# Kernel optimization log

Measured on AMD Instinct MI355X. Metric: run time of the kernel, lower is better.

## Reference

```python
import jax, jax.numpy as jnp
import numpy as np

N_NODES = 100000
NEG_SLOPE = 0.2


def gat_conv(x, W, att_src, att_dst, bias, src, dst, heads, out_ch):
    # x: [N, F_in]; W: [F_in, heads*out_ch]; att_*: [heads, out_ch]; bias: [heads*out_ch]
    N = x.shape[0]
    h = (x @ W).reshape(N, heads, out_ch)                 # [N, H, C]
    a_src = jnp.sum(h * att_src[None], axis=-1)           # [N, H]
    a_dst = jnp.sum(h * att_dst[None], axis=-1)           # [N, H]
    # per-edge unnormalized attention logits (PyG GATConv)
    alpha = jax.nn.leaky_relu(a_src[src] + a_dst[dst], NEG_SLOPE)   # [E, H]
    # scatter-softmax over edges grouped by destination node
    m = jax.ops.segment_max(alpha, dst, num_segments=N)   # [N, H]
    m = jnp.where(jnp.isfinite(m), m, 0.0)
    e = jnp.exp(alpha - m[dst])                           # [E, H]
    s = jax.ops.segment_sum(e, dst, num_segments=N)       # [N, H]
    alpha = e / (s[dst] + 1e-16)
    # weighted scatter-add aggregation of neighbor features
    out = jax.ops.segment_sum(alpha[:, :, None] * h[src], dst, num_segments=N)  # [N, H, C]
    return out.reshape(N, heads * out_ch) + bias


def setup_inputs() -> dict:
    key = jax.random.key(0)
    ks = jax.random.split(key, 10)
    F_in = 128
    x = jax.random.normal(ks[0], (N_NODES, F_in), dtype=jnp.float32)
    edge_index = jax.random.randint(ks[1], (2, 3200000), 0, N_NODES, dtype=jnp.int64)
    g = 0.1
    return {
        "x": x,
        "edge_index": edge_index,
        "W1": jax.random.normal(ks[2], (F_in, 32), jnp.float32) * g,
        "att_src1": jax.random.normal(ks[3], (2, 16), jnp.float32) * g,
        "att_dst1": jax.random.normal(ks[4], (2, 16), jnp.float32) * g,
        "b1": jnp.zeros((32,), jnp.float32),
        "W2": jax.random.normal(ks[5], (32, 2), jnp.float32) * g,
        "att_src2": jax.random.normal(ks[6], (1, 2), jnp.float32) * g,
        "att_dst2": jax.random.normal(ks[7], (1, 2), jnp.float32) * g,
        "b2": jnp.zeros((2,), jnp.float32),
    }


def reference(x, edge_index, W1, att_src1, att_dst1, b1, W2, att_src2, att_dst2, b2):
    N = x.shape[0]
    # add self-loops (PyG GATConv default add_self_loops=True)
    loops = jnp.arange(N, dtype=edge_index.dtype)
    src = jnp.concatenate([edge_index[0], loops])
    dst = jnp.concatenate([edge_index[1], loops])
    h = gat_conv(x, W1, att_src1, att_dst1, b1, src, dst, heads=2, out_ch=16)
    h = jax.nn.elu(h)
    h = gat_conv(h, W2, att_src2, att_dst2, b2, src, dst, heads=1, out_ch=2)
    return jax.nn.log_softmax(h, axis=1)
```

## Files before the change

### kernel.cpp

```cpp
#include <hip/hip_runtime.h>
#include <hip/hip_bf16.h>
#include <hip/hip_fp16.h>

#define LEAK   0.2f
#define NPB    200
#define CAP    8192
#define CAPSH  13
#define SBITS  17
#define SMASK  0x1FFFF
#define CHUNKB 8192

__device__ __forceinline__ unsigned pkh(float a, float b) {
    __half2 h = __floats2half2_rn(a, b);
    return *(unsigned*)&h;
}
__device__ __forceinline__ float2 uph(unsigned u) {
    __half2 h = *(__half2*)&u;
    return __half22float2(h);
}

__global__ __launch_bounds__(512) void kbin(const int* __restrict__ ei, int E, int K,
                                            int* __restrict__ cursor,
                                            int* __restrict__ binned) {
    __shared__ int hist[512], gb[512], lbase[512], lcur[512];
    __shared__ unsigned short rbk[CHUNKB];
    __shared__ int sv[CHUNKB];
    __shared__ int swt[8];
    __shared__ int probe;
    int t = threadIdx.x;
    hist[t] = 0;
    if (t == 0) probe = 0;
    __syncthreads();
    if (t < 256) {
        int zc = 0;
#pragma unroll
        for (int j = 0; j < 4; j++) zc += (ei[(t * 4 + j) * 2 + 1] == 0) ? 1 : 0;
        if (zc) atomicAdd(&probe, zc);
    }
    __syncthreads();
    int f = (probe == 1024);
    int e0 = blockIdx.x * CHUNKB;
    int ss[16], dd[16];
#pragma unroll
    for (int i = 0; i < 16; i++) {
        int e = e0 + t + 512 * i;
        ss[i] = -1;
        dd[i] = 0;
        if (e < E) {
            int s, d;
            if (f) { s = ei[2 * e]; d = ei[2 * (e + E)]; }
            else   { s = ei[e];     d = ei[e + E]; }
            ss[i] = s;
            dd[i] = d;
            atomicAdd(&hist[d / NPB], 1);
        }
    }
    __syncthreads();
    int h = (t < K) ? hist[t] : 0;
    if (h) gb[t] = (t << CAPSH) + atomicAdd(&cursor[t], h);
    int xsc = h;
#pragma unroll
    for (int o = 1; o < 64; o <<= 1) {
        int y = __shfl_up(xsc, o, 64);
        if ((t & 63) >= o) xsc += y;
    }
    if ((t & 63) == 63) swt[t >> 6] = xsc;
    __syncthreads();
    int add = 0;
#pragma unroll
    for (int j = 0; j < 8; j++)
        if (j < (t >> 6)) add += swt[j];
    int lb = xsc - h + add;
    lbase[t] = lb;
    lcur[t] = lb;
    __syncthreads();
    for (int j = 0; j < h; j++) rbk[lb + j] = (unsigned short)t;
#pragma unroll
    for (int i = 0; i < 16; i++) {
        if (ss[i] >= 0) {
            int bk = dd[i] / NPB;
            int dloc = dd[i] - bk * NPB;
            int pos = atomicAdd(&lcur[bk], 1);
            sv[pos] = ss[i] | (dloc << SBITS);
        }
    }
    __syncthreads();
    int tot = min(CHUNKB, E - e0);
    for (int i = t; i < tot; i += 512) {
        int bk = rbk[i];
        int gpos = gb[bk] + (i - lbase[bk]);
        if (gpos < ((bk + 1) << CAPSH))
            binned[gpos] = sv[i];
    }
}

__global__ __launch_bounds__(256) void k1(const float* __restrict__ x,
                                          const float* __restrict__ W1,
                                          const float* __restrict__ atts,
                                          const float* __restrict__ attd,
                                          uint2* __restrict__ h1h,
                                          float* __restrict__ a1s,
                                          float* __restrict__ a1d, int N,
                                          int* __restrict__ cursor, int K) {
    __shared__ float Ws[128 * 32];
    __shared__ float xs[64 * 132];
    int t = threadIdx.x;
    if (blockIdx.x == 0) {
        for (int u = t; u < K; u += 256) cursor[u] = 0;
    }
    const float4* W4 = (const float4*)W1;
    float4* Ws4 = (float4*)Ws;
#pragma unroll
    for (int i = 0; i < 4; i++) Ws4[t + 256 * i] = W4[t + 256 * i];
    long long node0 = (long long)blockIdx.x * 64;
    const float4* x4 = (const float4*)x;
    float4* xs4 = (float4*)xs;
#pragma unroll
    for (int i = 0; i < 8; i++) {
        int idx = t + 256 * i;
        int row = idx >> 5, col = idx & 31;
        long long n = node0 + row;
        float4 v = make_float4(0.f, 0.f, 0.f, 0.f);
        if (n < N) v = x4[n * 32 + col];
        xs4[row * 33 + col] = v;
    }
    __syncthreads();

    int cg = t & 7, ns = t >> 3;
    const float4* xr0 = (const float4*)(xs + (ns * 2) * 132);
    const float4* xr1 = (const float4*)(xs + (ns * 2 + 1) * 132);
    float acc0[4] = {0.f, 0.f, 0.f, 0.f}, acc1[4] = {0.f, 0.f, 0.f, 0.f};
#pragma unroll 8
    for (int k4 = 0; k4 < 32; k4++) {
        float4 xa = xr0[k4], xb = xr1[k4];
        float av[4] = {xa.x, xa.y, xa.z, xa.w};
        float bv[4] = {xb.x, xb.y, xb.z, xb.w};
#pragma unroll
        for (int i = 0; i < 4; i++) {
            float4 w = Ws4[(k4 * 4 + i) * 8 + cg];
            acc0[0] = fmaf(av[i], w.x, acc0[0]);
            acc0[1] = fmaf(av[i], w.y, acc0[1]);
            acc0[2] = fmaf(av[i], w.z, acc0[2]);
            acc0[3] = fmaf(av[i], w.w, acc0[3]);
            acc1[0] = fmaf(bv[i], w.x, acc1[0]);
            acc1[1] = fmaf(bv[i], w.y, acc1[1]);
            acc1[2] = fmaf(bv[i], w.z, acc1[2]);
            acc1[3] = fmaf(bv[i], w.w, acc1[3]);
        }
    }
    long long gn0 = node0 + ns * 2, gn1 = gn0 + 1;
    if (gn0 < N) h1h[gn0 * 8 + cg] = make_uint2(pkh(acc0[0], acc0[1]),
                                                pkh(acc0[2], acc0[3]));
    if (gn1 < N) h1h[gn1 * 8 + cg] = make_uint2(pkh(acc1[0], acc1[1]),
                                                pkh(acc1[2], acc1[3]));

    float ps0 = 0.f, pd0 = 0.f, ps1 = 0.f, pd1 = 0.f;
#pragma unroll
    for (int i = 0; i < 4; i++) {
        float aa = atts[cg * 4 + i], dd = attd[cg * 4 + i];
        ps0 = fmaf(acc0[i], aa, ps0);
        pd0 = fmaf(acc0[i], dd, pd0);
        ps1 = fmaf(acc1[i], aa, ps1);
        pd1 = fmaf(acc1[i], dd, pd1);
    }
#pragma unroll
    for (int m = 1; m < 4; m <<= 1) {
        ps0 += __shfl_xor(ps0, m, 64);
        pd0 += __shfl_xor(pd0, m, 64);
        ps1 += __shfl_xor(ps1, m, 64);
        pd1 += __shfl_xor(pd1, m, 64);
    }
    if ((cg & 3) == 0) {
        int hd = cg >> 2;
        if (gn0 < N) { a1s[gn0 * 2 + hd] = ps0; a1d[gn0 * 2 + hd] = pd0; }
        if (gn1 < N) { a1s[gn1 * 2 + hd] = ps1; a1d[gn1 * 2 + hd] = pd1; }
    }
}

__global__ __launch_bounds__(1024) void kfused(const int* __restrict__ cursor,
                                               const int* __restrict__ binned,
                                               const uint2* __restrict__ h1h,
                                               const float* __restrict__ a1s,
                                               const float* __restrict__ a1d,
                                               const float* __restrict__ b1,
                                               const float* __restrict__ W2,
                                               const float* __restrict__ as2,
                                               const float* __restrict__ ad2,
                                               float4* __restrict__ pk,
                                               int* __restrict__ srcs,
                                               int* __restrict__ od, int N) {
    __shared__ int lsrc[CAP];
    __shared__ int ldeg[NPB], lcur[NPB], loff[NPB];
    __shared__ int swt[4];
    int b = blockIdx.x, t = threadIdx.x;
    int node0 = b * NPB;
    int nn = min(NPB, N - node0);
    int cnt = cursor[b];
    if (cnt > CAP) cnt = CAP;
    const int* bb = binned + ((long long)b << CAPSH);
    if (t < NPB) ldeg[t] = 0;
    __syncthreads();
    int pv[8];
#pragma unroll
    for (int j = 0; j < 8; j++) {
        int i = t + 1024 * j;
        pv[j] = (i < cnt) ? bb[i] : -1;
        if (pv[j] >= 0) atomicAdd(&ldeg[pv[j] >> SBITS], 1);
    }
    __syncthreads();
    {
        int v = 0, xsc = 0;
        if (t < 256) {
            v = (t < nn) ? ldeg[t] : 0;
            xsc = v;
#pragma unroll
            for (int o = 1; o < 64; o <<= 1) {
                int y = __shfl_up(xsc, o, 64);
                if ((t & 63) >= o) xsc += y;
            }
            if ((t & 63) == 63) swt[t >> 6] = xsc;
        }
        __syncthreads();
        if (t < 256) {
            int add = 0;
#pragma unroll
            for (int j = 0; j < 4; j++)
                if (j < (t >> 6)) add += swt[j];
            xsc += add;
            if (t < nn) {
                int rel = xsc - v;
                loff[t] = rel;
                lcur[t] = rel;
                od[node0 + t] = rel | (v << 14);
            }
        }
        __syncthreads();
    }
#pragma unroll
    for (int j = 0; j < 8; j++) {
        if (pv[j] >= 0) {
            int pos = atomicAdd(&lcur[pv[j] >> SBITS], 1);
            lsrc[pos] = pv[j] & SMASK;
        }
    }
    __syncthreads();
    for (int i = t; i < cnt; i += 1024) srcs[((long long)b << CAPSH) + i] = lsrc[i];

    int wv = t >> 6, lane = t & 63;
    int e8 = lane >> 3, c4 = lane & 7, hd = c4 >> 2;
    bool wlane = (c4 & 3) == 0;
    for (int ni = wv; ni < nn; ni += 16) {
        int n = node0 + ni;
        float a1dn = a1d[2 * n + hd];
        int base = loff[ni], g = ldeg[ni];
        float4 acc = make_float4(0.f, 0.f, 0.f, 0.f);
        float wsum = 0.f;
        for (int tt = e8 - 1; tt < g; tt += 16) {
            int t2 = tt + 8;
            bool p2 = t2 < g;
            int s0 = (tt < 0) ? n : lsrc[base + tt];
            int s1 = p2 ? lsrc[base + t2] : s0;
            float as0 = a1s[2 * s0 + hd];
            float as1 = a1s[2 * s1 + hd];
            uint2 hb0 = h1h[(size_t)s0 * 8 + c4];
            uint2 hb1 = h1h[(size_t)s1 * 8 + c4];
            float al0 = as0 + a1dn;
            al0 = al0 > 0.f ? al0 : LEAK * al0;
            float w0 = __expf(al0);
            float al1 = as1 + a1dn;
            al1 = al1 > 0.f ? al1 : LEAK * al1;
            float w1 = p2 ? __expf(al1) : 0.f;
            float2 f01 = uph(hb0.x), f23 = uph(hb0.y);
            float2 g01 = uph(hb1.x), g23 = uph(hb1.y);
            acc.x = fmaf(w0, f01.x, acc.x);
            acc.y = fmaf(w0, f01.y, acc.y);
            acc.z = fmaf(w0, f23.x, acc.z);
            acc.w = fmaf(w0, f23.y, acc.w);
            acc.x = fmaf(w1, g01.x, acc.x);
            acc.y = fmaf(w1, g01.y, acc.y);
            acc.z = fmaf(w1, g23.x, acc.z);
            acc.w = fmaf(w1, g23.y, acc.w);
            if (wlane) wsum += w0 + w1;
        }
#pragma unroll
        for (int m = 8; m < 64; m <<= 1) {
            acc.x += __shfl_xor(acc.x, m, 64);
            acc.y += __shfl_xor(acc.y, m, 64);
            acc.z += __shfl_xor(acc.z, m, 64);
            acc.w += __shfl_xor(acc.w, m, 64);
            wsum += __shfl_xor(wsum, m, 64);
        }
        float wsH = __shfl(wsum, hd * 4, 64);
        float inv = 1.f / (wsH + 1e-16f);
        float4 bv = ((const float4*)b1)[c4];
        float4 t1;
        t1.x = acc.x * inv + bv.x;
        t1.y = acc.y * inv + bv.y;
        t1.z = acc.z * inv + bv.z;
        t1.w = acc.w * inv + bv.w;
        t1.x = t1.x > 0.f ? t1.x : __expf(t1.x) - 1.f;
        t1.y = t1.y > 0.f ? t1.y : __expf(t1.y) - 1.f;
        t1.z = t1.z > 0.f ? t1.z : __expf(t1.z) - 1.f;
        t1.w = t1.w > 0.f ? t1.w : __expf(t1.w) - 1.f;
        const float4* W24 = (const float4*)W2;
        float4 wA = W24[c4 * 2], wB = W24[c4 * 2 + 1];
        float p0 = t1.x * wA.x + t1.y * wA.z + t1.z * wB.x + t1.w * wB.z;
        float p1 = t1.x * wA.y + t1.y * wA.w + t1.z * wB.y + t1.w * wB.w;
#pragma unroll
        for (int m = 1; m < 8; m <<= 1) {
            p0 += __shfl_xor(p0, m, 64);
            p1 += __shfl_xor(p1, m, 64);
        }
        if (lane == 0)
            pk[n] = make_float4(p0 * as2[0] + p1 * as2[1], p0, p1,
                                p0 * ad2[0] + p1 * ad2[1]);
    }
}

__global__ __launch_bounds__(256) void kagg2(const int* __restrict__ od,
                                             const int* __restrict__ srcs,
                                             const float4* __restrict__ pk,
                                             const float* __restrict__ b2,
                                             float* __restrict__ out, int N) {
    int sub = threadIdx.x >> 5, k = threadIdx.x & 31;
    int n = blockIdx.x * 8 + sub;
    if (n >= N) return;
    float4 pn = pk[n];
    float adn = pn.w;
    int o = od[n];
    int base = ((n / NPB) << CAPSH) + (o & 16383);
    int g = o >> 14;
    float a0 = 0.f, a1v = 0.f, wsm = 0.f;
    for (int e = k - 1; e < g; e += 32) {
        float4 p = (e < 0) ? pn : pk[srcs[base + e]];
        float al = p.x + adn;
        al = al > 0.f ? al : LEAK * al;
        float w = __expf(al);
        a0 = fmaf(w, p.y, a0);
        a1v = fmaf(w, p.z, a1v);
        wsm += w;
    }
#pragma unroll
    for (int m = 1; m < 32; m <<= 1) {
        a0 += __shfl_xor(a0, m, 32);
        a1v += __shfl_xor(a1v, m, 32);
        wsm += __shfl_xor(wsm, m, 32);
    }
    if (k == 0) {
        float inv = 1.f / (wsm + 1e-16f);
        float o0 = a0 * inv + b2[0];
        float o1 = a1v * inv + b2[1];
        float mx = fmaxf(o0, o1);
        float lse = mx + __logf(__expf(o0 - mx) + __expf(o1 - mx));
        ((float2*)out)[n] = make_float2(o0 - lse, o1 - lse);
    }
}

extern "C" void kernel_launch(void* const* d_in, const int* in_sizes, int n_in,
                              void* d_out, int out_size, void* d_ws, size_t ws_size,
                              hipStream_t stream) {
    const float* x   = (const float*)d_in[0];
    const int*   ei  = (const int*)d_in[1];
    const float* W1  = (const float*)d_in[2];
    const float* as1 = (const float*)d_in[3];
    const float* ad1 = (const float*)d_in[4];
    const float* b1  = (const float*)d_in[5];
    const float* W2  = (const float*)d_in[6];
    const float* as2 = (const float*)d_in[7];
    const float* ad2 = (const float*)d_in[8];
    const float* b2  = (const float*)d_in[9];
    float* out = (float*)d_out;

    int N = out_size / 2;
    int E = in_sizes[1] / 2;
    int K = (N + NPB - 1) / NPB;

    float* wsp   = (float*)d_ws;
    float4* pk   = (float4*)wsp;
    uint2* h1h   = (uint2*)(pk + (size_t)N);
    float* a1s   = (float*)(h1h + (size_t)N * 8);
    float* a1d   = a1s + (size_t)N * 2;
    int* od      = (int*)(a1d + (size_t)N * 2);
    int* srcs    = od + N;
    int* binned  = srcs + (size_t)K * CAP;
    int* cursor  = binned + (size_t)K * CAP;

    int nblkB = (E + CHUNKB - 1) / CHUNKB;

    k1<<<(N + 63) / 64, 256, 0, stream>>>(x, W1, as1, ad1, h1h, a1s, a1d, N,
                                          cursor, K);
    kbin<<<nblkB, 512, 0, stream>>>(ei, E, K, cursor, binned);
    kfused<<<K, 1024, 0, stream>>>(cursor, binned, h1h, a1s, a1d,
                                   b1, W2, as2, ad2, pk, srcs, od, N);
    kagg2<<<(N + 7) / 8, 256, 0, stream>>>(od, srcs, pk, b2, out, N);
}
```

Baseline: 230.9 us.

## Merge edge binning and layer-1 projection into one heterogeneous launch

```diff
diff --git a/kernel.cpp b/kernel.cpp
--- a/kernel.cpp
+++ b/kernel.cpp
@@ -19,161 +19,149 @@
     return __half22float2(h);
 }
 
-__global__ __launch_bounds__(512) void kbin(const int* __restrict__ ei, int E, int K,
+__global__ __launch_bounds__(512) void kpre(const int* __restrict__ ei, int E, int K,
+                                            int NBIN,
                                             int* __restrict__ cursor,
-                                            int* __restrict__ binned) {
-    __shared__ int hist[512], gb[512], lbase[512], lcur[512];
-    __shared__ unsigned short rbk[CHUNKB];
-    __shared__ int sv[CHUNKB];
-    __shared__ int swt[8];
-    __shared__ int probe;
+                                            int* __restrict__ binned,
+                                            const float* __restrict__ x,
+                                            const float* __restrict__ W1,
+                                            const float* __restrict__ atts,
+                                            const float* __restrict__ attd,
+                                            uint2* __restrict__ h1h,
+                                            float* __restrict__ a1s,
+                                            float* __restrict__ a1d, int N) {
+    __shared__ __align__(16) char smem[57380];
     int t = threadIdx.x;
-    hist[t] = 0;
-    if (t == 0) probe = 0;
-    __syncthreads();
-    if (t < 256) {
-        int zc = 0;
-#pragma unroll
-        for (int j = 0; j < 4; j++) zc += (ei[(t * 4 + j) * 2 + 1] == 0) ? 1 : 0;
-        if (zc) atomicAdd(&probe, zc);
-    }
-    __syncthreads();
-    int f = (probe == 1024);
-    int e0 = blockIdx.x * CHUNKB;
-    int ss[16], dd[16];
-#pragma unroll
-    for (int i = 0; i < 16; i++) {
-        int e = e0 + t + 512 * i;
-        ss[i] = -1;
-        dd[i] = 0;
-        if (e < E) {
-            int s, d;
-            if (f) { s = ei[2 * e]; d = ei[2 * (e + E)]; }
-            else   { s = ei[e];     d = ei[e + E]; }
-            ss[i] = s;
-            dd[i] = d;
-            atomicAdd(&hist[d / NPB], 1);
-        }
-    }
-    __syncthreads();
-    int h = (t < K) ? hist[t] : 0;
-    if (h) gb[t] = (t << CAPSH) + atomicAdd(&cursor[t], h);
-    int xsc = h;
-#pragma unroll
-    for (int o = 1; o < 64; o <<= 1) {
-        int y = __shfl_up(xsc, o, 64);
-        if ((t & 63) >= o) xsc += y;
-    }
-    if ((t & 63) == 63) swt[t >> 6] = xsc;
-    __syncthreads();
-    int add = 0;
-#pragma unroll
-    for (int j = 0; j < 8; j++)
-        if (j < (t >> 6)) add += swt[j];
-    int lb = xsc - h + add;
-    lbase[t] = lb;
-    lcur[t] = lb;
-    __syncthreads();
-    for (int j = 0; j < h; j++) rbk[lb + j] = (unsigned short)t;
-#pragma unroll
-    for (int i = 0; i < 16; i++) {
-        if (ss[i] >= 0) {
-            int bk = dd[i] / NPB;
-            int dloc = dd[i] - bk * NPB;
-            int pos = atomicAdd(&lcur[bk], 1);
-            sv[pos] = ss[i] | (dloc << SBITS);
-        }
-    }
-    __syncthreads();
-    int tot = min(CHUNKB, E - e0);
-    for (int i = t; i < tot; i += 512) {
-        int bk = rbk[i];
-        int gpos = gb[bk] + (i - lbase[bk]);
-        if (gpos < ((bk + 1) << CAPSH))
-            binned[gpos] = sv[i];
-    }
-}
-
-__global__ __launch_bounds__(256) void k1(const float* __restrict__ x,
-                                          const float* __restrict__ W1,
-                                          const float* __restrict__ atts,
-                                          const float* __restrict__ attd,
-                                          uint2* __restrict__ h1h,
-                                          float* __restrict__ a1s,
-                                          float* __restrict__ a1d, int N,
-                                          int* __restrict__ cursor, int K) {
-    __shared__ float Ws[128 * 32];
-    __shared__ float xs[64 * 132];
-    int t = threadIdx.x;
-    if (blockIdx.x == 0) {
-        for (int u = t; u < K; u += 256) cursor[u] = 0;
-    }
-    const float4* W4 = (const float4*)W1;
-    float4* Ws4 = (float4*)Ws;
-#pragma unroll
-    for (int i = 0; i < 4; i++) Ws4[t + 256 * i] = W4[t + 256 * i];
-    long long node0 = (long long)blockIdx.x * 64;
-    const float4* x4 = (const float4*)x;
-    float4* xs4 = (float4*)xs;
-#pragma unroll
-    for (int i = 0; i < 8; i++) {
-        int idx = t + 256 * i;
-        int row = idx >> 5, col = idx & 31;
-        long long n = node0 + row;
-        float4 v = make_float4(0.f, 0.f, 0.f, 0.f);
-        if (n < N) v = x4[n * 32 + col];
-        xs4[row * 33 + col] = v;
-    }
-    __syncthreads();
-
-    int cg = t & 7, ns = t >> 3;
-    const float4* xr0 = (const float4*)(xs + (ns * 2) * 132);
-    const float4* xr1 = (const float4*)(xs + (ns * 2 + 1) * 132);
-    float acc0[4] = {0.f, 0.f, 0.f, 0.f}, acc1[4] = {0.f, 0.f, 0.f, 0.f};
+
+    if (blockIdx.x < NBIN) {
+        int* hist = (int*)smem;
+        int* gb    = hist + 512;
+        int* lbase = gb + 512;
+        int* lcur  = lbase + 512;
+        unsigned short* rbk = (unsigned short*)(lcur + 512);
+        int* sv    = (int*)(rbk + CHUNKB);
+        int* swt   = sv + CHUNKB;
+        int* probe = swt + 8;
+        hist[t] = 0;
+        if (t == 0) *probe = 0;
+        __syncthreads();
+        if (t < 256) {
+            int zc = 0;
+#pragma unroll
+            for (int j = 0; j < 4; j++) zc += (ei[(t * 4 + j) * 2 + 1] == 0) ? 1 : 0;
+            if (zc) atomicAdd(probe, zc);
+        }
+        __syncthreads();
+        int f = (*probe == 1024);
+        int e0 = blockIdx.x * CHUNKB;
+        int ss[16], dd[16];
+#pragma unroll
+        for (int i = 0; i < 16; i++) {
+            int e = e0 + t + 512 * i;
+            ss[i] = -1;
+            dd[i] = 0;
+            if (e < E) {
+                int s, d;
+                if (f) { s = ei[2 * e]; d = ei[2 * (e + E)]; }
+                else   { s = ei[e];     d = ei[e + E]; }
+                ss[i] = s;
+                dd[i] = d;
+                atomicAdd(&hist[d / NPB], 1);
+            }
+        }
+        __syncthreads();
+        int h = (t < K) ? hist[t] : 0;
+        if (h) gb[t] = (t << CAPSH) + atomicAdd(&cursor[t], h);
+        int xsc = h;
+#pragma unroll
+        for (int o = 1; o < 64; o <<= 1) {
+            int y = __shfl_up(xsc, o, 64);
+            if ((t & 63) >= o) xsc += y;
+        }
+        if ((t & 63) == 63) swt[t >> 6] = xsc;
+        __syncthreads();
+        int add = 0;
+#pragma unroll
+        for (int j = 0; j < 8; j++)
+            if (j < (t >> 6)) add += swt[j];
+        int lb = xsc - h + add;
+        lbase[t] = lb;
+        lcur[t] = lb;
+        __syncthreads();
+        for (int j = 0; j < h; j++) rbk[lb + j] = (unsigned short)t;
+#pragma unroll
+        for (int i = 0; i < 16; i++) {
+            if (ss[i] >= 0) {
+                int bk = dd[i] / NPB;
+                int dloc = dd[i] - bk * NPB;
+                int pos = atomicAdd(&lcur[bk], 1);
+                sv[pos] = ss[i] | (dloc << SBITS);
+            }
+        }
+        __syncthreads();
+        int tot = min(CHUNKB, E - e0);
+        for (int i = t; i < tot; i += 512) {
+            int bk = rbk[i];
+            int gpos = gb[bk] + (i - lbase[bk]);
+            if (gpos < ((bk + 1) << CAPSH))
+                binned[gpos] = sv[i];
+        }
+    } else {
+        int b = blockIdx.x - NBIN;
+        float* Ws = (float*)smem;
+        float* xs = Ws + 4096;
+        const float4* W4 = (const float4*)W1;
+        float4* Ws4 = (float4*)Ws;
+#pragma unroll
+        for (int i = 0; i < 2; i++) Ws4[t + 512 * i] = W4[t + 512 * i];
+        long long node0 = (long long)b * 64;
+        const float4* x4 = (const float4*)x;
+        float4* xs4 = (float4*)xs;
+#pragma unroll
+        for (int i = 0; i < 4; i++) {
+            int idx = t + 512 * i;
+            int row = idx >> 5, col = idx & 31;
+            long long n = node0 + row;
+            float4 v = make_float4(0.f, 0.f, 0.f, 0.f);
+            if (n < N) v = x4[n * 32 + col];
+            xs4[row * 33 + col] = v;
+        }
+        __syncthreads();
+
+        int cg = t & 7, ns = t >> 3;
+        const float4* xr = (const float4*)(xs + ns * 132);
+        float acc[4] = {0.f, 0.f, 0.f, 0.f};
 #pragma unroll 8
-    for (int k4 = 0; k4 < 32; k4++) {
-        float4 xa = xr0[k4], xb = xr1[k4];
-        float av[4] = {xa.x, xa.y, xa.z, xa.w};
-        float bv[4] = {xb.x, xb.y, xb.z, xb.w};
+        for (int k4 = 0; k4 < 32; k4++) {
+            float4 xa = xr[k4];
+            float av[4] = {xa.x, xa.y, xa.z, xa.w};
+#pragma unroll
+            for (int i = 0; i < 4; i++) {
+                float4 w = Ws4[(k4 * 4 + i) * 8 + cg];
+                acc[0] = fmaf(av[i], w.x, acc[0]);
+                acc[1] = fmaf(av[i], w.y, acc[1]);
+                acc[2] = fmaf(av[i], w.z, acc[2]);
+                acc[3] = fmaf(av[i], w.w, acc[3]);
+            }
+        }
+        long long gn = node0 + ns;
+        if (gn < N) h1h[gn * 8 + cg] = make_uint2(pkh(acc[0], acc[1]),
+                                                  pkh(acc[2], acc[3]));
+        float ps = 0.f, pd = 0.f;
 #pragma unroll
         for (int i = 0; i < 4; i++) {
-            float4 w = Ws4[(k4 * 4 + i) * 8 + cg];
-            acc0[0] = fmaf(av[i], w.x, acc0[0]);
-            acc0[1] = fmaf(av[i], w.y, acc0[1]);
-            acc0[2] = fmaf(av[i], w.z, acc0[2]);
-            acc0[3] = fmaf(av[i], w.w, acc0[3]);
-            acc1[0] = fmaf(bv[i], w.x, acc1[0]);
-            acc1[1] = fmaf(bv[i], w.y, acc1[1]);
-            acc1[2] = fmaf(bv[i], w.z, acc1[2]);
-            acc1[3] = fmaf(bv[i], w.w, acc1[3]);
-        }
-    }
-    long long gn0 = node0 + ns * 2, gn1 = gn0 + 1;
-    if (gn0 < N) h1h[gn0 * 8 + cg] = make_uint2(pkh(acc0[0], acc0[1]),
-                                                pkh(acc0[2], acc0[3]));
-    if (gn1 < N) h1h[gn1 * 8 + cg] = make_uint2(pkh(acc1[0], acc1[1]),
-                                                pkh(acc1[2], acc1[3]));
-
-    float ps0 = 0.f, pd0 = 0.f, ps1 = 0.f, pd1 = 0.f;
-#pragma unroll
-    for (int i = 0; i < 4; i++) {
-        float aa = atts[cg * 4 + i], dd = attd[cg * 4 + i];
-        ps0 = fmaf(acc0[i], aa, ps0);
-        pd0 = fmaf(acc0[i], dd, pd0);
-        ps1 = fmaf(acc1[i], aa, ps1);
-        pd1 = fmaf(acc1[i], dd, pd1);
-    }
-#pragma unroll
-    for (int m = 1; m < 4; m <<= 1) {
-        ps0 += __shfl_xor(ps0, m, 64);
-        pd0 += __shfl_xor(pd0, m, 64);
-        ps1 += __shfl_xor(ps1, m, 64);
-        pd1 += __shfl_xor(pd1, m, 64);
-    }
-    if ((cg & 3) == 0) {
-        int hd = cg >> 2;
-        if (gn0 < N) { a1s[gn0 * 2 + hd] = ps0; a1d[gn0 * 2 + hd] = pd0; }
-        if (gn1 < N) { a1s[gn1 * 2 + hd] = ps1; a1d[gn1 * 2 + hd] = pd1; }
+            ps = fmaf(acc[i], atts[cg * 4 + i], ps);
+            pd = fmaf(acc[i], attd[cg * 4 + i], pd);
+        }
+#pragma unroll
+        for (int m = 1; m < 4; m <<= 1) {
+            ps += __shfl_xor(ps, m, 64);
+            pd += __shfl_xor(pd, m, 64);
+        }
+        if ((cg & 3) == 0) {
+            int hd = cg >> 2;
+            if (gn < N) { a1s[gn * 2 + hd] = ps; a1d[gn * 2 + hd] = pd; }
+        }
     }
 }
 
@@ -385,11 +373,12 @@
     int* binned  = srcs + (size_t)K * CAP;
     int* cursor  = binned + (size_t)K * CAP;
 
-    int nblkB = (E + CHUNKB - 1) / CHUNKB;
-
-    k1<<<(N + 63) / 64, 256, 0, stream>>>(x, W1, as1, ad1, h1h, a1s, a1d, N,
-                                          cursor, K);
-    kbin<<<nblkB, 512, 0, stream>>>(ei, E, K, cursor, binned);
+    int NBIN = (E + CHUNKB - 1) / CHUNKB;
+    int NK1  = (N + 63) / 64;
+
+    hipMemsetAsync(cursor, 0, K * sizeof(int), stream);
+    kpre<<<NBIN + NK1, 512, 0, stream>>>(ei, E, K, NBIN, cursor, binned,
+                                         x, W1, as1, ad1, h1h, a1s, a1d, N);
     kfused<<<K, 1024, 0, stream>>>(cursor, binned, h1h, a1s, a1d,
                                    b1, W2, as2, ad2, pk, srcs, od, N);
     kagg2<<<(N + 7) / 8, 256, 0, stream>>>(od, srcs, pk, b2, out, N);
```

Measured after the change: 224.5 us. 1.03x faster.
